# Kernel optimization log

Measured on AMD Instinct MI355X. Metric: run time of the kernel, lower is better.

Reference implementation:

```python
import jax, jax.numpy as jnp
import numpy as np
import math

# config mirrors init_kwargs
PATCH = 16      # PatchSize
HDIM = 64       # Headhdim
N = 256         # image side
C = 16          # nchann (must be divisible by 4 for the 2D PE)
B = 16          # batch
RANK = 3
NPATCH = N // PATCH


def _pe2d(height, width, d_model):
    """2D sinusoidal positional encoding, (height, width, d_model)."""
    dq = d_model // 4
    div = np.exp(np.arange(dq, dtype=np.float32) * (-math.log(10000.0) / dq))
    px = np.arange(height, dtype=np.float32)[:, None, None] * div  # (H,1,dq)
    py = np.arange(width, dtype=np.float32)[None, :, None] * div   # (1,W,dq)
    pe_x = np.zeros((height, width, d_model // 2), np.float32)
    pe_y = np.zeros((height, width, d_model // 2), np.float32)
    pe_x[:, :, 0::2] = np.sin(px)
    pe_x[:, :, 1::2] = np.cos(px)
    pe_y[:, :, 0::2] = np.sin(py)
    pe_y[:, :, 1::2] = np.cos(py)
    return np.concatenate([pe_x, pe_y], axis=-1)


def setup_inputs() -> dict:
    key = jax.random.key(0)
    ks = jax.random.split(key, 9)
    pp = PATCH * PATCH
    kin = NPATCH * HDIM
    s_tok = 1.0 / math.sqrt(pp)
    s_proj = 1.0 / math.sqrt(kin)
    pos_enc = jnp.asarray(_pe2d(N, N, C).transpose(2, 0, 1))[None]  # (1,C,N,N)
    return {
        "x": jax.random.normal(ks[0], (B, C, N, N), jnp.float32),
        "pos_enc": pos_enc,
        "Wv": jax.random.normal(ks[1], (HDIM, pp), jnp.float32) * s_tok,
        "bv": jax.random.normal(ks[2], (HDIM,), jnp.float32) * s_tok,
        "Wh": jax.random.normal(ks[3], (HDIM, pp), jnp.float32) * s_tok,
        "bh": jax.random.normal(ks[4], (HDIM,), jnp.float32) * s_tok,
        "Vw": jax.random.normal(ks[5], (RANK, N, kin), jnp.float32) * s_proj,
        "Vb": jax.random.normal(ks[6], (RANK, N), jnp.float32) * s_proj,
        "Hw": jax.random.normal(ks[7], (RANK, N, kin), jnp.float32) * s_proj,
        "Hb": jax.random.normal(ks[8], (RANK, N), jnp.float32) * s_proj,
    }


def reference(x, pos_enc, Wv, bv, Wh, bh, Vw, Vb, Hw, Hb):
    b, c, h, w = x.shape
    p = PATCH
    npc = h // p  # npatch
    d = Wv.shape[0]
    y = x + pos_enc
    # unfold(2,p,p).unfold(3,p,p).view(b,c,np,np,p*p)
    patches = (y.reshape(b, c, npc, p, npc, p)
                 .transpose(0, 1, 2, 4, 3, 5)
                 .reshape(b, c, npc, npc, p * p))
    # token projections applied to every patch; linearity lets us project once
    vt = jnp.einsum('bcjik,dk->bcjid', patches, Wv) + bv  # (b,c,j,i,d)
    ht = jnp.einsum('bcjik,dk->bcjid', patches, Wh) + bh
    # original sums Linear outputs over j (for V) / over i (for H),
    # which also accumulates the bias npatch times -- preserved here.
    vcomp = vt.sum(axis=2).reshape(b, c, npc * d)  # concat over i
    hcomp = ht.sum(axis=3).reshape(b, c, npc * d)  # concat over j
    V = jnp.einsum('bck,rnk->bcnr', vcomp, Vw) + Vb.T  # (b,c,N,rank)
    H = jnp.einsum('bck,rnk->bcnr', hcomp, Hw) + Hb.T
    return jnp.einsum('bcnr,bcmr->bcnm', V, H)  # low-rank V @ H^T per (b,c)
```

## Files before the change

### kernel.cpp

```cpp
#include <hip/hip_runtime.h>

#define KIN 1024

__device__ __forceinline__ float4 f4add(float4 a, float4 b) {
    return make_float4(a.x + b.x, a.y + b.y, a.z + b.z, a.w + b.w);
}
__device__ __forceinline__ float f4dot(float4 a, float4 b) {
    return a.x * b.x + a.y * b.y + a.z * b.z + a.w * b.w;
}
__device__ __forceinline__ unsigned short f2bf(float f) {
    unsigned int u = __float_as_uint(f);
    u += 0x7FFFu + ((u >> 16) & 1u);
    return (unsigned short)(u >> 16);
}

typedef __attribute__((ext_vector_type(8))) short bf16x8;
typedef __attribute__((ext_vector_type(4))) float f32x4;

__global__ __launch_bounds__(256) void k1_fused(
    const float* __restrict__ x, const float* __restrict__ pe,
    const float* __restrict__ Wv, const float* __restrict__ Wh,
    const float* __restrict__ Vw, const float* __restrict__ Hw,
    float4* __restrict__ Wqv, float4* __restrict__ Wqh,
    unsigned short* __restrict__ Vw_bf, unsigned short* __restrict__ Hw_bf,
    float* __restrict__ colsum_buf, float* __restrict__ rowsum_buf)
{
    const int blk = blockIdx.x, t = threadIdx.x;

    if (blk < 16) {
        int idx = blk * 256 + t;
        int kq = idx >> 6, d = idx & 63;
        Wqv[idx] = *(const float4*)(Wv + d * 256 + 4 * kq);
        Wqh[idx] = *(const float4*)(Wh + d * 256 + 4 * kq);
        return;
    }

    if (blk >= 4368) {
        const int idx = blk - 4368;
        #pragma unroll
        for (int rr = 0; rr < 2; ++rr) {
            const int row = 2 * idx + rr;
            const float4* src = (const float4*)((row < 768)
                ? (Vw + (size_t)row * 1024)
                : (Hw + (size_t)(row - 768) * 1024));
            unsigned short* dst = ((row < 768) ? Vw_bf + (size_t)row * 1024
                                               : Hw_bf + (size_t)(row - 768) * 1024);
            float4 v = src[t];
            ushort4 o = make_ushort4(f2bf(v.x), f2bf(v.y), f2bf(v.z), f2bf(v.w));
            ((ushort4*)dst)[t] = o;
        }
        return;
    }

    __shared__ float srow[16][264];
    __shared__ float cpart[4][256];

    const int b2 = blk - 16;
    const int img = b2 >> 4, pr = b2 & 15;
    const float* ib = (img < 256) ? (x + (size_t)img * 65536)
                                  : (pe + (size_t)(img - 256) * 65536);
    const int w = t >> 6, l = t & 63;

    float4 v[4];
    const float* base = ib + (size_t)(pr + 64 * w) * 256 + 4 * l;
    #pragma unroll
    for (int j = 0; j < 4; ++j)
        v[j] = *(const float4*)(base + j * 4096);

    *(float4*)&cpart[w][4 * l] = f4add(f4add(v[0], v[1]), f4add(v[2], v[3]));

    #pragma unroll
    for (int j = 0; j < 4; ++j)
        *(float4*)&srow[4 * w + j][4 * l] = v[j];
    __syncthreads();

    {
        const int lr = t >> 4, pc = t & 15;
        float s = 0.f;
        #pragma unroll
        for (int i = 0; i < 16; ++i) s += srow[lr][pc + 16 * i];
        const int grow = pr + 16 * lr;
        rowsum_buf[(size_t)img * 4096 + grow * 16 + pc] = s;
    }
    {
        colsum_buf[(size_t)img * 4096 + pr * 256 + t] =
            cpart[0][t] + cpart[1][t] + cpart[2][t] + cpart[3][t];
    }
}

__global__ __launch_bounds__(1024) void k1c(
    const float* __restrict__ colsum_buf, const float* __restrict__ rowsum_buf,
    const float4* __restrict__ Wqv, const float4* __restrict__ Wqh,
    const float* __restrict__ bv, const float* __restrict__ bh,
    unsigned short* __restrict__ vcomp_bf, unsigned short* __restrict__ hcomp_bf)
{
    __shared__ float cs[16][256];
    __shared__ float rs[256][16];
    __shared__ float vp[8][1024];
    __shared__ float hp[8][1024];

    const int bc = blockIdx.x, c = bc & 15, t = threadIdx.x;

    {
        float4 a = ((const float4*)(colsum_buf + (size_t)bc * 4096))[t];
        float4 p = ((const float4*)(colsum_buf + (size_t)(256 + c) * 4096))[t];
        ((float4*)cs)[t] = f4add(a, p);
        float4 b = ((const float4*)(rowsum_buf + (size_t)bc * 4096))[t];
        float4 q = ((const float4*)(rowsum_buf + (size_t)(256 + c) * 4096))[t];
        ((float4*)rs)[t] = f4add(b, q);
    }
    __syncthreads();

    const int w = t >> 6, l = t & 63;
    if (w < 8) {
        const int kq0 = w * 8;
        float acc[16];
        #pragma unroll
        for (int s = 0; s < 16; ++s) acc[s] = 0.f;
        #pragma unroll 2
        for (int kq = kq0; kq < kq0 + 8; ++kq) {
            float4 wq = Wqv[kq * 64 + l];
            const int pr = kq >> 2, pc4 = (kq & 3) * 4;
            #pragma unroll
            for (int s = 0; s < 16; ++s)
                acc[s] += f4dot(wq, *(const float4*)&cs[pr][s * 16 + pc4]);
        }
        #pragma unroll
        for (int s = 0; s < 16; ++s) vp[w][s * 64 + l] = acc[s];
    } else {
        const int kq0 = (w - 8) * 8;
        float acc[16];
        #pragma unroll
        for (int s = 0; s < 16; ++s) acc[s] = 0.f;
        #pragma unroll 2
        for (int kq = kq0; kq < kq0 + 8; ++kq) {
            float4 wq = Wqh[kq * 64 + l];
            const int pr = kq >> 2, pc4 = (kq & 3) * 4;
            #pragma unroll
            for (int s = 0; s < 16; ++s)
                acc[s] += f4dot(wq, *(const float4*)&rs[s * 16 + pr][pc4]);
        }
        #pragma unroll
        for (int s = 0; s < 16; ++s) hp[w - 8][s * 64 + l] = acc[s];
    }
    __syncthreads();

    {
        float v = 0.f, hsum = 0.f;
        #pragma unroll
        for (int k = 0; k < 8; ++k) { v += vp[k][t]; hsum += hp[k][t]; }
        vcomp_bf[(size_t)bc * KIN + t] = f2bf(v + 16.f * bv[t & 63]);
        hcomp_bf[(size_t)bc * KIN + t] = f2bf(hsum + 16.f * bh[t & 63]);
    }
}

__global__ __launch_bounds__(256) void k2_mfma(
    const unsigned short* __restrict__ vcomp_bf,
    const unsigned short* __restrict__ hcomp_bf,
    const unsigned short* __restrict__ Vw_bf,
    const unsigned short* __restrict__ Hw_bf,
    float* __restrict__ Vp, float* __restrict__ Hp, int KSplit, int KC)
{
    __shared__ unsigned short As[64][136];
    __shared__ unsigned short Bs[64][136];

    const int mat = blockIdx.z;
    const unsigned short* A = mat ? hcomp_bf : vcomp_bf;
    const unsigned short* B = mat ? Hw_bf : Vw_bf;
    float*                P = mat ? Hp : Vp;

    const int rn0 = blockIdx.x * 64;
    const int bct = blockIdx.y / KSplit, ks = blockIdx.y % KSplit;
    const int bc0 = bct * 64;
    const int t = threadIdx.x, w = t >> 6, l = t & 63;

    f32x4 acc[4];
    #pragma unroll
    for (int nf = 0; nf < 4; ++nf) acc[nf] = (f32x4)(0.f);

    const int nch = KC >> 7;
    for (int ch = 0; ch < nch; ++ch) {
        const int k0 = ks * KC + ch * 128;
        #pragma unroll
        for (int j = 0; j < 4; ++j) {
            const int idx = t + j * 256;
            const int row = idx >> 4, c16 = idx & 15;
            uint4 va = *(const uint4*)(A + (size_t)(bc0 + row) * KIN + k0 + c16 * 8);
            *(uint4*)&As[row][c16 * 8] = va;
            uint4 vb = *(const uint4*)(B + (size_t)(rn0 + row) * KIN + k0 + c16 * 8);
            *(uint4*)&Bs[row][c16 * 8] = vb;
        }
        __syncthreads();

        #pragma unroll
        for (int kst = 0; kst < 4; ++kst) {
            const int kl = kst * 32 + (l >> 4) * 8;
            bf16x8 a = *(const bf16x8*)&As[w * 16 + (l & 15)][kl];
            #pragma unroll
            for (int nf = 0; nf < 4; ++nf) {
                bf16x8 b = *(const bf16x8*)&Bs[nf * 16 + (l & 15)][kl];
                acc[nf] = __builtin_amdgcn_mfma_f32_16x16x32_bf16(a, b, acc[nf], 0, 0, 0);
            }
        }
        __syncthreads();
    }

    const int r = rn0 >> 8;
    const int nbase = rn0 & 255;
    #pragma unroll
    for (int nf = 0; nf < 4; ++nf) {
        const int n = nbase + nf * 16 + (l & 15);
        #pragma unroll
        for (int q = 0; q < 4; ++q) {
            const int m = (l >> 4) * 4 + q;
            const int bc = bc0 + w * 16 + m;
            P[(((size_t)ks * 256 + bc) * 3 + r) * 256 + n] = acc[nf][q];
        }
    }
}

__global__ __launch_bounds__(256) void k3_outer(
    const float* __restrict__ Vp, const float* __restrict__ Hp,
    const float* __restrict__ Vb, const float* __restrict__ Hb,
    float* __restrict__ out, int KSplit)
{
    __shared__ float sh[3][256];
    __shared__ float sv[3][128];

    const int bc = blockIdx.y, nt = blockIdx.x, t = threadIdx.x;

    #pragma unroll
    for (int r = 0; r < 3; ++r) {
        float a = Hb[r * 256 + t];
        for (int ks = 0; ks < KSplit; ++ks)
            a += Hp[(((size_t)ks * 256 + bc) * 3 + r) * 256 + t];
        sh[r][t] = a;
    }
    for (int idx = t; idx < 384; idx += 256) {
        int r = idx >> 7, nn = idx & 127;
        float a = Vb[r * 256 + nt * 128 + nn];
        for (int ks = 0; ks < KSplit; ++ks)
            a += Vp[(((size_t)ks * 256 + bc) * 3 + r) * 256 + nt * 128 + nn];
        sv[r][nn] = a;
    }
    __syncthreads();

    const float h0 = sh[0][t], h1 = sh[1][t], h2 = sh[2][t];
    float* ob = out + ((size_t)bc * 256 + nt * 128) * 256;
    #pragma unroll 4
    for (int nn = 0; nn < 128; ++nn)
        ob[nn * 256 + t] = sv[0][nn] * h0 + sv[1][nn] * h1 + sv[2][nn] * h2;
}

extern "C" void kernel_launch(void* const* d_in, const int* in_sizes, int n_in,
                              void* d_out, int out_size, void* d_ws, size_t ws_size,
                              hipStream_t stream)
{
    const float* x  = (const float*)d_in[0];
    const float* pe = (const float*)d_in[1];
    const float* Wv = (const float*)d_in[2];
    const float* bv = (const float*)d_in[3];
    const float* Wh = (const float*)d_in[4];
    const float* bh = (const float*)d_in[5];
    const float* Vw = (const float*)d_in[6];
    const float* Vb = (const float*)d_in[7];
    const float* Hw = (const float*)d_in[8];
    const float* Hb = (const float*)d_in[9];
    float* out = (float*)d_out;

    float* ws          = (float*)d_ws;
    float* wqv         = ws;
    float* wqh         = ws + 16384;
    float* colsum_buf  = ws + 32768;
    float* rowsum_buf  = ws + 1146880;
    unsigned short* vcomp_bf = (unsigned short*)(ws + 2260992);
    unsigned short* hcomp_bf = (unsigned short*)(ws + 2392064);
    unsigned short* Vw_bf    = (unsigned short*)(ws + 2523136);
    unsigned short* Hw_bf    = (unsigned short*)(ws + 2916352);
    float* rest        = ws + 3309568;

    int KS = 1;
    if      (ws_size >= (3309568ull + 8 * 393216ull) * 4) KS = 8;
    else if (ws_size >= (3309568ull + 4 * 393216ull) * 4) KS = 4;
    else if (ws_size >= (3309568ull + 2 * 393216ull) * 4) KS = 2;
    const int KC = KIN / KS;

    float* Vp = rest;
    float* Hp = rest + (size_t)KS * 196608;

    k1_fused<<<16 + 4352 + 768, 256, 0, stream>>>(
        x, pe, Wv, Wh, Vw, Hw, (float4*)wqv, (float4*)wqh,
        Vw_bf, Hw_bf, colsum_buf, rowsum_buf);
    k1c<<<256, 1024, 0, stream>>>(colsum_buf, rowsum_buf,
                                  (const float4*)wqv, (const float4*)wqh,
                                  bv, bh, vcomp_bf, hcomp_bf);
    k2_mfma<<<dim3(12, 4 * KS, 2), 256, 0, stream>>>(
        vcomp_bf, hcomp_bf, Vw_bf, Hw_bf, Vp, Hp, KS, KC);
    k3_outer<<<dim3(2, 256), 256, 0, stream>>>(Vp, Hp, Vb, Hb, out, KS);
}
```

Baseline: 55.52 us.

## Compose token and low-rank projection weights into a single K=4096 GEMM

Precomputes composed weights (Vw·Wv and Hw·Wh) with MFMA in a new kernel and folds the token biases into effective output biases. The separate k1c token-projection stage disappears, and the main GEMM runs directly on the bf16 patch column and row sums with K=4096, adding the positional-encoding sums while staging tiles. The main GEMM's N tile grows to 128. This removes one kernel and the intermediate comp buffers, but the main GEMM now has four times the K depth and larger weight reads, and the weight composition is recomputed on every call.

New measurement: 97.88 us. 1.76x slower.

```diff
diff --git a/kernel.cpp b/kernel.cpp
--- a/kernel.cpp
+++ b/kernel.cpp
@@ -1,65 +1,123 @@
 #include <hip/hip_runtime.h>
 
-#define KIN 1024
+#define KIN4 4096
 
 __device__ __forceinline__ float4 f4add(float4 a, float4 b) {
     return make_float4(a.x + b.x, a.y + b.y, a.z + b.z, a.w + b.w);
-}
-__device__ __forceinline__ float f4dot(float4 a, float4 b) {
-    return a.x * b.x + a.y * b.y + a.z * b.z + a.w * b.w;
 }
 __device__ __forceinline__ unsigned short f2bf(float f) {
     unsigned int u = __float_as_uint(f);
     u += 0x7FFFu + ((u >> 16) & 1u);
     return (unsigned short)(u >> 16);
 }
+__device__ __forceinline__ float bf2f(unsigned int u) {
+    return __uint_as_float((u & 0xFFFFu) << 16);
+}
+__device__ __forceinline__ unsigned int pack2(float a, float b) {
+    return (unsigned int)f2bf(a) | ((unsigned int)f2bf(b) << 16);
+}
 
 typedef __attribute__((ext_vector_type(8))) short bf16x8;
 typedef __attribute__((ext_vector_type(4))) float f32x4;
 
-__global__ __launch_bounds__(256) void k1_fused(
-    const float* __restrict__ x, const float* __restrict__ pe,
+__global__ __launch_bounds__(256) void k0_compose(
     const float* __restrict__ Wv, const float* __restrict__ Wh,
     const float* __restrict__ Vw, const float* __restrict__ Hw,
-    float4* __restrict__ Wqv, float4* __restrict__ Wqh,
-    unsigned short* __restrict__ Vw_bf, unsigned short* __restrict__ Hw_bf,
-    float* __restrict__ colsum_buf, float* __restrict__ rowsum_buf)
+    const float* __restrict__ bv, const float* __restrict__ bh,
+    const float* __restrict__ Vb, const float* __restrict__ Hb,
+    unsigned short* __restrict__ vwe, unsigned short* __restrict__ hwe,
+    float* __restrict__ vbias_eff, float* __restrict__ hbias_eff)
 {
     const int blk = blockIdx.x, t = threadIdx.x;
 
-    if (blk < 16) {
-        int idx = blk * 256 + t;
-        int kq = idx >> 6, d = idx & 63;
-        Wqv[idx] = *(const float4*)(Wv + d * 256 + 4 * kq);
-        Wqh[idx] = *(const float4*)(Wh + d * 256 + 4 * kq);
+    if (blk >= 384) {
+        const int i = blk - 384;
+        const int mat = i / 3, grp = i % 3;
+        const int rn = grp * 256 + t;
+        const float* W = (mat ? Hw : Vw) + (size_t)rn * 1024;
+        const float* bb = mat ? bh : bv;
+        float acc = 0.f;
+        #pragma unroll 4
+        for (int kq = 0; kq < 256; ++kq) {
+            float4 w4 = *(const float4*)(W + 4 * kq);
+            float4 b4 = *(const float4*)(bb + ((4 * kq) & 63));
+            acc += w4.x * b4.x + w4.y * b4.y + w4.z * b4.z + w4.w * b4.w;
+        }
+        const float base = (mat ? Hb : Vb)[rn];
+        (mat ? hbias_eff : vbias_eff)[rn] = base + 16.f * acc;
         return;
     }
 
-    if (blk >= 4368) {
-        const int idx = blk - 4368;
-        #pragma unroll
-        for (int rr = 0; rr < 2; ++rr) {
-            const int row = 2 * idx + rr;
-            const float4* src = (const float4*)((row < 768)
-                ? (Vw + (size_t)row * 1024)
-                : (Hw + (size_t)(row - 768) * 1024));
-            unsigned short* dst = ((row < 768) ? Vw_bf + (size_t)row * 1024
-                                               : Hw_bf + (size_t)(row - 768) * 1024);
-            float4 v = src[t];
-            ushort4 o = make_ushort4(f2bf(v.x), f2bf(v.y), f2bf(v.z), f2bf(v.w));
-            ((ushort4*)dst)[t] = o;
-        }
-        return;
-    }
-
+    __shared__ unsigned short As[64][88];
+    __shared__ unsigned short Bs[128][88];
+
+    const int mat = blk / 192;
+    const int rem = blk - mat * 192;
+    const int seg = rem / 12, rnt = rem % 12;
+    const int rn0 = rnt * 64;
+    const float* A  = mat ? Hw : Vw;
+    const float* Wm = mat ? Wh : Wv;
+    unsigned short* E = mat ? hwe : vwe;
+
+    const int w = t >> 6, l = t & 63;
+
+    for (int g = t; g < 512; g += 256) {
+        const int row = g >> 3, d8 = (g & 7) * 8;
+        const float* src = A + (size_t)(rn0 + row) * 1024 + seg * 64 + d8;
+        float4 v0 = *(const float4*)src, v1 = *(const float4*)(src + 4);
+        uint4 o;
+        o.x = pack2(v0.x, v0.y); o.y = pack2(v0.z, v0.w);
+        o.z = pack2(v1.x, v1.y); o.w = pack2(v1.z, v1.w);
+        *(uint4*)&As[row][d8] = o;
+    }
+
+    for (int ph = 0; ph < 2; ++ph) {
+        __syncthreads();
+        for (int idx = t; idx < 2048; idx += 256) {
+            const int d = idx >> 5, pq = idx & 31;
+            float4 v = *(const float4*)(Wm + d * 256 + ph * 128 + pq * 4);
+            Bs[pq * 4 + 0][d] = f2bf(v.x);
+            Bs[pq * 4 + 1][d] = f2bf(v.y);
+            Bs[pq * 4 + 2][d] = f2bf(v.z);
+            Bs[pq * 4 + 3][d] = f2bf(v.w);
+        }
+        __syncthreads();
+
+        #pragma unroll
+        for (int prl = 0; prl < 8; ++prl) {
+            f32x4 acc = (f32x4)(0.f);
+            #pragma unroll
+            for (int kst = 0; kst < 2; ++kst) {
+                const int kl = kst * 32 + (l >> 4) * 8;
+                bf16x8 a = *(const bf16x8*)&As[w * 16 + (l & 15)][kl];
+                bf16x8 b = *(const bf16x8*)&Bs[prl * 16 + (l & 15)][kl];
+                acc = __builtin_amdgcn_mfma_f32_16x16x32_bf16(a, b, acc, 0, 0, 0);
+            }
+            const int pr = ph * 8 + prl, pc = l & 15;
+            const int col = (mat ? (seg * 256 + pr * 16) : (pr * 256 + seg * 16)) + pc;
+            #pragma unroll
+            for (int q = 0; q < 4; ++q) {
+                const int rn = rn0 + w * 16 + (l >> 4) * 4 + q;
+                E[(size_t)rn * KIN4 + col] = f2bf(acc[q]);
+            }
+        }
+    }
+}
+
+__global__ __launch_bounds__(256) void k1_reduce(
+    const float* __restrict__ x, const float* __restrict__ pe,
+    unsigned short* __restrict__ cs_bf, unsigned short* __restrict__ rs_bf,
+    float* __restrict__ pe_cs, float* __restrict__ pe_rs)
+{
     __shared__ float srow[16][264];
     __shared__ float cpart[4][256];
 
-    const int b2 = blk - 16;
-    const int img = b2 >> 4, pr = b2 & 15;
-    const float* ib = (img < 256) ? (x + (size_t)img * 65536)
-                                  : (pe + (size_t)(img - 256) * 65536);
-    const int w = t >> 6, l = t & 63;
+    const int blk = blockIdx.x;
+    const int img = blk >> 4, pr = blk & 15;
+    const bool isX = img < 256;
+    const float* ib = isX ? (x + (size_t)img * 65536)
+                          : (pe + (size_t)(img - 256) * 65536);
+    const int t = threadIdx.x, w = t >> 6, l = t & 63;
 
     float4 v[4];
     const float* base = ib + (size_t)(pr + 64 * w) * 256 + 4 * l;
@@ -80,115 +138,64 @@
         #pragma unroll
         for (int i = 0; i < 16; ++i) s += srow[lr][pc + 16 * i];
         const int grow = pr + 16 * lr;
-        rowsum_buf[(size_t)img * 4096 + grow * 16 + pc] = s;
+        if (isX) rs_bf[(size_t)img * KIN4 + grow * 16 + pc] = f2bf(s);
+        else     pe_rs[(size_t)(img - 256) * KIN4 + grow * 16 + pc] = s;
     }
     {
-        colsum_buf[(size_t)img * 4096 + pr * 256 + t] =
-            cpart[0][t] + cpart[1][t] + cpart[2][t] + cpart[3][t];
-    }
-}
-
-__global__ __launch_bounds__(1024) void k1c(
-    const float* __restrict__ colsum_buf, const float* __restrict__ rowsum_buf,
-    const float4* __restrict__ Wqv, const float4* __restrict__ Wqh,
-    const float* __restrict__ bv, const float* __restrict__ bh,
-    unsigned short* __restrict__ vcomp_bf, unsigned short* __restrict__ hcomp_bf)
-{
-    __shared__ float cs[16][256];
-    __shared__ float rs[256][16];
-    __shared__ float vp[8][1024];
-    __shared__ float hp[8][1024];
-
-    const int bc = blockIdx.x, c = bc & 15, t = threadIdx.x;
-
-    {
-        float4 a = ((const float4*)(colsum_buf + (size_t)bc * 4096))[t];
-        float4 p = ((const float4*)(colsum_buf + (size_t)(256 + c) * 4096))[t];
-        ((float4*)cs)[t] = f4add(a, p);
-        float4 b = ((const float4*)(rowsum_buf + (size_t)bc * 4096))[t];
-        float4 q = ((const float4*)(rowsum_buf + (size_t)(256 + c) * 4096))[t];
-        ((float4*)rs)[t] = f4add(b, q);
-    }
-    __syncthreads();
-
-    const int w = t >> 6, l = t & 63;
-    if (w < 8) {
-        const int kq0 = w * 8;
-        float acc[16];
-        #pragma unroll
-        for (int s = 0; s < 16; ++s) acc[s] = 0.f;
-        #pragma unroll 2
-        for (int kq = kq0; kq < kq0 + 8; ++kq) {
-            float4 wq = Wqv[kq * 64 + l];
-            const int pr = kq >> 2, pc4 = (kq & 3) * 4;
-            #pragma unroll
-            for (int s = 0; s < 16; ++s)
-                acc[s] += f4dot(wq, *(const float4*)&cs[pr][s * 16 + pc4]);
-        }
-        #pragma unroll
-        for (int s = 0; s < 16; ++s) vp[w][s * 64 + l] = acc[s];
-    } else {
-        const int kq0 = (w - 8) * 8;
-        float acc[16];
-        #pragma unroll
-        for (int s = 0; s < 16; ++s) acc[s] = 0.f;
-        #pragma unroll 2
-        for (int kq = kq0; kq < kq0 + 8; ++kq) {
-            float4 wq = Wqh[kq * 64 + l];
-            const int pr = kq >> 2, pc4 = (kq & 3) * 4;
-            #pragma unroll
-            for (int s = 0; s < 16; ++s)
-                acc[s] += f4dot(wq, *(const float4*)&rs[s * 16 + pr][pc4]);
-        }
-        #pragma unroll
-        for (int s = 0; s < 16; ++s) hp[w - 8][s * 64 + l] = acc[s];
-    }
-    __syncthreads();
-
-    {
-        float v = 0.f, hsum = 0.f;
-        #pragma unroll
-        for (int k = 0; k < 8; ++k) { v += vp[k][t]; hsum += hp[k][t]; }
-        vcomp_bf[(size_t)bc * KIN + t] = f2bf(v + 16.f * bv[t & 63]);
-        hcomp_bf[(size_t)bc * KIN + t] = f2bf(hsum + 16.f * bh[t & 63]);
+        const float s = cpart[0][t] + cpart[1][t] + cpart[2][t] + cpart[3][t];
+        if (isX) cs_bf[(size_t)img * KIN4 + pr * 256 + t] = f2bf(s);
+        else     pe_cs[(size_t)(img - 256) * KIN4 + pr * 256 + t] = s;
     }
 }
 
 __global__ __launch_bounds__(256) void k2_mfma(
-    const unsigned short* __restrict__ vcomp_bf,
-    const unsigned short* __restrict__ hcomp_bf,
-    const unsigned short* __restrict__ Vw_bf,
-    const unsigned short* __restrict__ Hw_bf,
+    const unsigned short* __restrict__ cs_bf, const unsigned short* __restrict__ rs_bf,
+    const float* __restrict__ pe_cs, const float* __restrict__ pe_rs,
+    const unsigned short* __restrict__ vwe, const unsigned short* __restrict__ hwe,
     float* __restrict__ Vp, float* __restrict__ Hp, int KSplit, int KC)
 {
     __shared__ unsigned short As[64][136];
-    __shared__ unsigned short Bs[64][136];
+    __shared__ unsigned short Bs[128][136];
 
     const int mat = blockIdx.z;
-    const unsigned short* A = mat ? hcomp_bf : vcomp_bf;
-    const unsigned short* B = mat ? Hw_bf : Vw_bf;
+    const unsigned short* A = mat ? rs_bf : cs_bf;
+    const float*         PE = mat ? pe_rs : pe_cs;
+    const unsigned short* B = mat ? hwe : vwe;
     float*                P = mat ? Hp : Vp;
 
-    const int rn0 = blockIdx.x * 64;
+    const int rn0 = blockIdx.x * 128;
     const int bct = blockIdx.y / KSplit, ks = blockIdx.y % KSplit;
     const int bc0 = bct * 64;
     const int t = threadIdx.x, w = t >> 6, l = t & 63;
 
-    f32x4 acc[4];
-    #pragma unroll
-    for (int nf = 0; nf < 4; ++nf) acc[nf] = (f32x4)(0.f);
+    f32x4 acc[8];
+    #pragma unroll
+    for (int nf = 0; nf < 8; ++nf) acc[nf] = (f32x4)(0.f);
 
     const int nch = KC >> 7;
     for (int ch = 0; ch < nch; ++ch) {
         const int k0 = ks * KC + ch * 128;
         #pragma unroll
-        for (int j = 0; j < 4; ++j) {
-            const int idx = t + j * 256;
-            const int row = idx >> 4, c16 = idx & 15;
-            uint4 va = *(const uint4*)(A + (size_t)(bc0 + row) * KIN + k0 + c16 * 8);
-            *(uint4*)&As[row][c16 * 8] = va;
-            uint4 vb = *(const uint4*)(B + (size_t)(rn0 + row) * KIN + k0 + c16 * 8);
-            *(uint4*)&Bs[row][c16 * 8] = vb;
+        for (int g0 = 0; g0 < 4; ++g0) {
+            const int g = t + g0 * 256;
+            const int row = g >> 4, c8 = (g & 15) * 8;
+            const int c = (bc0 + row) & 15;
+            uint4 va = *(const uint4*)(A + (size_t)(bc0 + row) * KIN4 + k0 + c8);
+            float4 p0 = *(const float4*)(PE + (size_t)c * KIN4 + k0 + c8);
+            float4 p1 = *(const float4*)(PE + (size_t)c * KIN4 + k0 + c8 + 4);
+            uint4 o;
+            o.x = pack2(bf2f(va.x) + p0.x, bf2f(va.x >> 16) + p0.y);
+            o.y = pack2(bf2f(va.y) + p0.z, bf2f(va.y >> 16) + p0.w);
+            o.z = pack2(bf2f(va.z) + p1.x, bf2f(va.z >> 16) + p1.y);
+            o.w = pack2(bf2f(va.w) + p1.z, bf2f(va.w >> 16) + p1.w);
+            *(uint4*)&As[row][c8] = o;
+        }
+        #pragma unroll
+        for (int g0 = 0; g0 < 8; ++g0) {
+            const int g = t + g0 * 256;
+            const int row = g >> 4, c8 = (g & 15) * 8;
+            *(uint4*)&Bs[row][c8] =
+                *(const uint4*)(B + (size_t)(rn0 + row) * KIN4 + k0 + c8);
         }
         __syncthreads();
 
@@ -197,7 +204,7 @@
             const int kl = kst * 32 + (l >> 4) * 8;
             bf16x8 a = *(const bf16x8*)&As[w * 16 + (l & 15)][kl];
             #pragma unroll
-            for (int nf = 0; nf < 4; ++nf) {
+            for (int nf = 0; nf < 8; ++nf) {
                 bf16x8 b = *(const bf16x8*)&Bs[nf * 16 + (l & 15)][kl];
                 acc[nf] = __builtin_amdgcn_mfma_f32_16x16x32_bf16(a, b, acc[nf], 0, 0, 0);
             }
@@ -205,15 +212,13 @@
         __syncthreads();
     }
 
-    const int r = rn0 >> 8;
-    const int nbase = rn0 & 255;
-    #pragma unroll
-    for (int nf = 0; nf < 4; ++nf) {
-        const int n = nbase + nf * 16 + (l & 15);
+    #pragma unroll
+    for (int nf = 0; nf < 8; ++nf) {
+        const int rn = rn0 + nf * 16 + (l & 15);
+        const int r = rn >> 8, n = rn & 255;
         #pragma unroll
         for (int q = 0; q < 4; ++q) {
-            const int m = (l >> 4) * 4 + q;
-            const int bc = bc0 + w * 16 + m;
+            const int bc = bc0 + w * 16 + (l >> 4) * 4 + q;
             P[(((size_t)ks * 256 + bc) * 3 + r) * 256 + n] = acc[nf][q];
         }
     }
@@ -268,33 +273,31 @@
     const float* Hb = (const float*)d_in[9];
     float* out = (float*)d_out;
 
-    float* ws          = (float*)d_ws;
-    float* wqv         = ws;
-    float* wqh         = ws + 16384;
-    float* colsum_buf  = ws + 32768;
-    float* rowsum_buf  = ws + 1146880;
-    unsigned short* vcomp_bf = (unsigned short*)(ws + 2260992);
-    unsigned short* hcomp_bf = (unsigned short*)(ws + 2392064);
-    unsigned short* Vw_bf    = (unsigned short*)(ws + 2523136);
-    unsigned short* Hw_bf    = (unsigned short*)(ws + 2916352);
-    float* rest        = ws + 3309568;
+    float* ws = (float*)d_ws;
+    unsigned short* vwe   = (unsigned short*)ws;
+    unsigned short* hwe   = (unsigned short*)(ws + 1572864);
+    unsigned short* cs_bf = (unsigned short*)(ws + 3145728);
+    unsigned short* rs_bf = (unsigned short*)(ws + 3670016);
+    float* pe_cs      = ws + 4194304;
+    float* pe_rs      = ws + 4259840;
+    float* vbias_eff  = ws + 4325376;
+    float* hbias_eff  = ws + 4326400;
+    float* rest       = ws + 4327424;
 
     int KS = 1;
-    if      (ws_size >= (3309568ull + 8 * 393216ull) * 4) KS = 8;
-    else if (ws_size >= (3309568ull + 4 * 393216ull) * 4) KS = 4;
-    else if (ws_size >= (3309568ull + 2 * 393216ull) * 4) KS = 2;
-    const int KC = KIN / KS;
+    if      (ws_size >= (4327424ull + 8 * 393216ull) * 4) KS = 8;
+    else if (ws_size >= (4327424ull + 4 * 393216ull) * 4) KS = 4;
+    else if (ws_size >= (4327424ull + 2 * 393216ull) * 4) KS = 2;
+    const int KC = KIN4 / KS;
 
     float* Vp = rest;
     float* Hp = rest + (size_t)KS * 196608;
 
-    k1_fused<<<16 + 4352 + 768, 256, 0, stream>>>(
-        x, pe, Wv, Wh, Vw, Hw, (float4*)wqv, (float4*)wqh,
-        Vw_bf, Hw_bf, colsum_buf, rowsum_buf);
-    k1c<<<256, 1024, 0, stream>>>(colsum_buf, rowsum_buf,
-                                  (const float4*)wqv, (const float4*)wqh,
-                                  bv, bh, vcomp_bf, hcomp_bf);
-    k2_mfma<<<dim3(12, 4 * KS, 2), 256, 0, stream>>>(
-        vcomp_bf, hcomp_bf, Vw_bf, Hw_bf, Vp, Hp, KS, KC);
-    k3_outer<<<dim3(2, 256), 256, 0, stream>>>(Vp, Hp, Vb, Hb, out, KS);
-}
+    k0_compose<<<390, 256, 0, stream>>>(Wv, Wh, Vw, Hw, bv, bh, Vb, Hb,
+                                        vwe, hwe, vbias_eff, hbias_eff);
+    k1_reduce<<<4352, 256, 0, stream>>>(x, pe, cs_bf, rs_bf, pe_cs, pe_rs);
+    k2_mfma<<<dim3(6, 4 * KS, 2), 256, 0, stream>>>(
+        cs_bf, rs_bf, pe_cs, pe_rs, vwe, hwe, Vp, Hp, KS, KC);
+    k3_outer<<<dim3(2, 256), 256, 0, stream>>>(Vp, Hp, vbias_eff, hbias_eff,
+                                               out, KS);
+}
```

## Replace scalar token projection kernel with bf16 MFMA GEMM

Applied to the files above, without the earlier changes.

The second stage, which projects summed patch rows and columns through Wv/Wh, moves from per-(b,c) FP32 dot-product blocks of 1024 threads to a batched bf16 MFMA GEMM tiled over 64 images by 64 outputs per segment. Wv/Wh are now pre-converted to bf16 instead of being repacked as float4. The intent is to use matrix cores and drop the shared-memory partial reduction. In exchange, the projection inputs are rounded to bf16, which loses some precision, and the grid shrinks to 128 blocks.

After: 55.37 us. About the same (-0.3%).

```diff
diff --git a/kernel.cpp b/kernel.cpp
--- a/kernel.cpp
+++ b/kernel.cpp
@@ -4,15 +4,15 @@
 
 __device__ __forceinline__ float4 f4add(float4 a, float4 b) {
     return make_float4(a.x + b.x, a.y + b.y, a.z + b.z, a.w + b.w);
-}
-__device__ __forceinline__ float f4dot(float4 a, float4 b) {
-    return a.x * b.x + a.y * b.y + a.z * b.z + a.w * b.w;
 }
 __device__ __forceinline__ unsigned short f2bf(float f) {
     unsigned int u = __float_as_uint(f);
     u += 0x7FFFu + ((u >> 16) & 1u);
     return (unsigned short)(u >> 16);
 }
+__device__ __forceinline__ unsigned int pack2(float a, float b) {
+    return (unsigned int)f2bf(a) | ((unsigned int)f2bf(b) << 16);
+}
 
 typedef __attribute__((ext_vector_type(8))) short bf16x8;
 typedef __attribute__((ext_vector_type(4))) float f32x4;
@@ -21,17 +21,23 @@
     const float* __restrict__ x, const float* __restrict__ pe,
     const float* __restrict__ Wv, const float* __restrict__ Wh,
     const float* __restrict__ Vw, const float* __restrict__ Hw,
-    float4* __restrict__ Wqv, float4* __restrict__ Wqh,
+    unsigned short* __restrict__ wv_bf, unsigned short* __restrict__ wh_bf,
     unsigned short* __restrict__ Vw_bf, unsigned short* __restrict__ Hw_bf,
     float* __restrict__ colsum_buf, float* __restrict__ rowsum_buf)
 {
     const int blk = blockIdx.x, t = threadIdx.x;
 
     if (blk < 16) {
-        int idx = blk * 256 + t;
-        int kq = idx >> 6, d = idx & 63;
-        Wqv[idx] = *(const float4*)(Wv + d * 256 + 4 * kq);
-        Wqh[idx] = *(const float4*)(Wh + d * 256 + 4 * kq);
+        const int idx = blk * 256 + t;
+        const int mat = idx >> 11, rem = idx & 2047;
+        const int d = rem >> 5, c8 = (rem & 31) * 8;
+        const float* W = mat ? Wh : Wv;
+        float4 v0 = *(const float4*)(W + d * 256 + c8);
+        float4 v1 = *(const float4*)(W + d * 256 + c8 + 4);
+        uint4 o;
+        o.x = pack2(v0.x, v0.y); o.y = pack2(v0.z, v0.w);
+        o.z = pack2(v1.x, v1.y); o.w = pack2(v1.z, v1.w);
+        *(uint4*)((mat ? wh_bf : wv_bf) + d * 256 + c8) = o;
         return;
     }
 
@@ -88,69 +94,78 @@
     }
 }
 
-__global__ __launch_bounds__(1024) void k1c(
+__global__ __launch_bounds__(256) void k1c_mfma(
     const float* __restrict__ colsum_buf, const float* __restrict__ rowsum_buf,
-    const float4* __restrict__ Wqv, const float4* __restrict__ Wqh,
+    const unsigned short* __restrict__ wv_bf, const unsigned short* __restrict__ wh_bf,
     const float* __restrict__ bv, const float* __restrict__ bh,
     unsigned short* __restrict__ vcomp_bf, unsigned short* __restrict__ hcomp_bf)
 {
-    __shared__ float cs[16][256];
-    __shared__ float rs[256][16];
-    __shared__ float vp[8][1024];
-    __shared__ float hp[8][1024];
-
-    const int bc = blockIdx.x, c = bc & 15, t = threadIdx.x;
+    __shared__ unsigned short As[64][264];
+    __shared__ unsigned short Bs[64][264];
+
+    const int seg = blockIdx.x;
+    const int bc0 = blockIdx.y * 64;
+    const int mat = blockIdx.z;
+    const float* S = mat ? rowsum_buf : colsum_buf;
+    const unsigned short* Wbf = mat ? wh_bf : wv_bf;
+    const float* bb = mat ? bh : bv;
+    unsigned short* dst = mat ? hcomp_bf : vcomp_bf;
+
+    const int t = threadIdx.x, w = t >> 6, l = t & 63;
 
     {
-        float4 a = ((const float4*)(colsum_buf + (size_t)bc * 4096))[t];
-        float4 p = ((const float4*)(colsum_buf + (size_t)(256 + c) * 4096))[t];
-        ((float4*)cs)[t] = f4add(a, p);
-        float4 b = ((const float4*)(rowsum_buf + (size_t)bc * 4096))[t];
-        float4 q = ((const float4*)(rowsum_buf + (size_t)(256 + c) * 4096))[t];
-        ((float4*)rs)[t] = f4add(b, q);
+        const int row = t >> 2, kq0 = (t & 3) * 64;
+        const float* bx = S + (size_t)(bc0 + row) * 4096;
+        const float* bp = S + (size_t)(256 + ((bc0 + row) & 15)) * 4096;
+        #pragma unroll
+        for (int f = 0; f < 8; ++f) {
+            const int k2 = kq0 + f * 8;
+            const int off = mat ? (seg * 256 + k2)
+                                : ((k2 >> 4) * 256 + seg * 16 + (k2 & 15));
+            float4 x0 = *(const float4*)(bx + off);
+            float4 x1 = *(const float4*)(bx + off + 4);
+            float4 p0 = *(const float4*)(bp + off);
+            float4 p1 = *(const float4*)(bp + off + 4);
+            uint4 o;
+            o.x = pack2(x0.x + p0.x, x0.y + p0.y);
+            o.y = pack2(x0.z + p0.z, x0.w + p0.w);
+            o.z = pack2(x1.x + p1.x, x1.y + p1.y);
+            o.w = pack2(x1.z + p1.z, x1.w + p1.w);
+            *(uint4*)&As[row][k2] = o;
+        }
+    }
+    #pragma unroll
+    for (int j = 0; j < 8; ++j) {
+        const int idx = t + j * 256;
+        const int d = idx >> 5, c8 = (idx & 31) * 8;
+        *(uint4*)&Bs[d][c8] = *(const uint4*)(Wbf + d * 256 + c8);
     }
     __syncthreads();
 
-    const int w = t >> 6, l = t & 63;
-    if (w < 8) {
-        const int kq0 = w * 8;
-        float acc[16];
-        #pragma unroll
-        for (int s = 0; s < 16; ++s) acc[s] = 0.f;
-        #pragma unroll 2
-        for (int kq = kq0; kq < kq0 + 8; ++kq) {
-            float4 wq = Wqv[kq * 64 + l];
-            const int pr = kq >> 2, pc4 = (kq & 3) * 4;
-            #pragma unroll
-            for (int s = 0; s < 16; ++s)
-                acc[s] += f4dot(wq, *(const float4*)&cs[pr][s * 16 + pc4]);
-        }
-        #pragma unroll
-        for (int s = 0; s < 16; ++s) vp[w][s * 64 + l] = acc[s];
-    } else {
-        const int kq0 = (w - 8) * 8;
-        float acc[16];
-        #pragma unroll
-        for (int s = 0; s < 16; ++s) acc[s] = 0.f;
-        #pragma unroll 2
-        for (int kq = kq0; kq < kq0 + 8; ++kq) {
-            float4 wq = Wqh[kq * 64 + l];
-            const int pr = kq >> 2, pc4 = (kq & 3) * 4;
-            #pragma unroll
-            for (int s = 0; s < 16; ++s)
-                acc[s] += f4dot(wq, *(const float4*)&rs[s * 16 + pr][pc4]);
-        }
-        #pragma unroll
-        for (int s = 0; s < 16; ++s) hp[w - 8][s * 64 + l] = acc[s];
-    }
-    __syncthreads();
-
-    {
-        float v = 0.f, hsum = 0.f;
-        #pragma unroll
-        for (int k = 0; k < 8; ++k) { v += vp[k][t]; hsum += hp[k][t]; }
-        vcomp_bf[(size_t)bc * KIN + t] = f2bf(v + 16.f * bv[t & 63]);
-        hcomp_bf[(size_t)bc * KIN + t] = f2bf(hsum + 16.f * bh[t & 63]);
+    f32x4 acc[4];
+    #pragma unroll
+    for (int nf = 0; nf < 4; ++nf) acc[nf] = (f32x4)(0.f);
+
+    #pragma unroll
+    for (int kst = 0; kst < 8; ++kst) {
+        const int kl = kst * 32 + (l >> 4) * 8;
+        bf16x8 a = *(const bf16x8*)&As[w * 16 + (l & 15)][kl];
+        #pragma unroll
+        for (int nf = 0; nf < 4; ++nf) {
+            bf16x8 b = *(const bf16x8*)&Bs[nf * 16 + (l & 15)][kl];
+            acc[nf] = __builtin_amdgcn_mfma_f32_16x16x32_bf16(a, b, acc[nf], 0, 0, 0);
+        }
+    }
+
+    #pragma unroll
+    for (int nf = 0; nf < 4; ++nf) {
+        const int d = nf * 16 + (l & 15);
+        const float bias = 16.f * bb[d];
+        #pragma unroll
+        for (int q = 0; q < 4; ++q) {
+            const int bc = bc0 + w * 16 + (l >> 4) * 4 + q;
+            dst[(size_t)bc * KIN + seg * 64 + d] = f2bf(acc[nf][q] + bias);
+        }
     }
 }
 
@@ -268,32 +283,31 @@
     const float* Hb = (const float*)d_in[9];
     float* out = (float*)d_out;
 
-    float* ws          = (float*)d_ws;
-    float* wqv         = ws;
-    float* wqh         = ws + 16384;
-    float* colsum_buf  = ws + 32768;
-    float* rowsum_buf  = ws + 1146880;
-    unsigned short* vcomp_bf = (unsigned short*)(ws + 2260992);
-    unsigned short* hcomp_bf = (unsigned short*)(ws + 2392064);
-    unsigned short* Vw_bf    = (unsigned short*)(ws + 2523136);
-    unsigned short* Hw_bf    = (unsigned short*)(ws + 2916352);
-    float* rest        = ws + 3309568;
+    float* ws = (float*)d_ws;
+    unsigned short* wv_bf = (unsigned short*)ws;
+    unsigned short* wh_bf = (unsigned short*)(ws + 8192);
+    float* colsum_buf  = ws + 16384;
+    float* rowsum_buf  = ws + 1130496;
+    unsigned short* vcomp_bf = (unsigned short*)(ws + 2244608);
+    unsigned short* hcomp_bf = (unsigned short*)(ws + 2375680);
+    unsigned short* Vw_bf    = (unsigned short*)(ws + 2506752);
+    unsigned short* Hw_bf    = (unsigned short*)(ws + 2899968);
+    float* rest        = ws + 3293184;
 
     int KS = 1;
-    if      (ws_size >= (3309568ull + 8 * 393216ull) * 4) KS = 8;
-    else if (ws_size >= (3309568ull + 4 * 393216ull) * 4) KS = 4;
-    else if (ws_size >= (3309568ull + 2 * 393216ull) * 4) KS = 2;
+    if      (ws_size >= (3293184ull + 8 * 393216ull) * 4) KS = 8;
+    else if (ws_size >= (3293184ull + 4 * 393216ull) * 4) KS = 4;
+    else if (ws_size >= (3293184ull + 2 * 393216ull) * 4) KS = 2;
     const int KC = KIN / KS;
 
     float* Vp = rest;
     float* Hp = rest + (size_t)KS * 196608;
 
     k1_fused<<<16 + 4352 + 768, 256, 0, stream>>>(
-        x, pe, Wv, Wh, Vw, Hw, (float4*)wqv, (float4*)wqh,
+        x, pe, Wv, Wh, Vw, Hw, wv_bf, wh_bf,
         Vw_bf, Hw_bf, colsum_buf, rowsum_buf);
-    k1c<<<256, 1024, 0, stream>>>(colsum_buf, rowsum_buf,
-                                  (const float4*)wqv, (const float4*)wqh,
-                                  bv, bh, vcomp_bf, hcomp_bf);
+    k1c_mfma<<<dim3(16, 4, 2), 256, 0, stream>>>(
+        colsum_buf, rowsum_buf, wv_bf, wh_bf, bv, bh, vcomp_bf, hcomp_bf);
     k2_mfma<<<dim3(12, 4 * KS, 2), 256, 0, stream>>>(
         vcomp_bf, hcomp_bf, Vw_bf, Hw_bf, Vp, Hp, KS, KC);
     k3_outer<<<dim3(2, 256), 256, 0, stream>>>(Vp, Hp, Vb, Hb, out, KS);
```
